# Kernel optimization log

Hardware: AMD Instinct MI355X
Metric: run time of the kernel (lower is better)

## Reference

```python
import jax, jax.numpy as jnp
import numpy as np

N_COARSE = 262145   # GMGN self.n
K_LEVELS = 5        # self.k
M_NBR = 9           # self.m
HID = 2048          # hidden_channels


def _build_grid():
    # replicates GMGN.init_toep_kernel (mtype='toep_mg')
    n_fine = 2 * (N_COARSE - 1) + 1          # 524289
    x = np.linspace(-1.0, 1.0, n_fine)
    x_lst, idx_lst = [], []
    for _ in range(K_LEVELS):
        n = x.shape[0]
        idx = np.arange((n - 1) // 2 - M_NBR + 1, (n - 1) // 2 + M_NBR)[1::2]  # m-1 center pts
        idx_lst.append(idx)
        x_lst.append(x[idx])
        x = x[::2]                            # injection1d
    x_lst.append(x)                           # coarse grid
    xs = np.concatenate(x_lst)[:, None].astype(np.float32)   # (N_eval, 1)
    nbrs = np.stack(idx_lst[::-1]).astype(np.int64)          # (k, m-1), coarse->fine
    return xs, nbrs


def setup_inputs() -> dict:
    key = jax.random.key(0)
    xs_np, nbrs_np = _build_grid()
    dims = [1, HID, HID, HID, HID, 1]
    inp = {"xs": jnp.asarray(xs_np), "nbrs": jnp.asarray(nbrs_np), "k": K_LEVELS, "m": M_NBR}
    ks = jax.random.split(key, 10)
    for j in range(5):
        bd = 1.0 / np.sqrt(dims[j])           # nn.Linear default init range
        inp[f"w{j}"] = jax.random.uniform(ks[2 * j], (dims[j], dims[j + 1]), jnp.float32, -bd, bd)
        inp[f"b{j}"] = jax.random.uniform(ks[2 * j + 1], (dims[j + 1],), jnp.float32, -bd, bd)
    return inp


def _interp1d(a):
    # linear prolongation: (n,) -> (2n-1,); even slots copy, odd slots average
    out = jnp.zeros((2 * a.shape[0] - 1,), a.dtype)
    out = out.at[0::2].set(a)
    return out.at[1::2].set(0.5 * (a[:-1] + a[1:]))


def _forward(xs, Ws, bs, nbrs, k, m):
    h = xs
    for W, b in zip(Ws, bs):
        h = jax.nn.relu(h @ W + b)            # MLP appends relu after every Linear (incl. last)
    Amg = h[:, 0]                             # (N_eval,) pointwise kernel values
    band = m - 1
    Abands = [Amg[band * i: band * (i + 1)] for i in range(k)][::-1]
    Ah = Amg[band * k:]                       # coarse kernel, length (n0-1)/2^k + 1
    for i in range(k):
        Ah = _interp1d(Ah)                    # upsample one level
        Ah = Ah.at[nbrs[i]].set(Abands[i])    # overwrite center band with exact MLP evals
    return Ah[None, None]                     # (1, 1, 2*(n-1)+1)


def reference(xs, w0, b0, w1, b1, w2, b2, w3, b3, w4, b4, nbrs, k, m):
    return _forward(xs, (w0, w1, w2, w3, w4), (b0, b1, b2, b3, b4), nbrs, k, m)
```

## Files before the change

### kernel.cpp

```cpp
#include <hip/hip_runtime.h>
#include <stdint.h>

#define HID    2048
#define MPTS   16425
#define MTILES 129
#define NTIL   16
#define KTIL   64
#define BIMG   5120

typedef float    f32x4 __attribute__((ext_vector_type(4)));
typedef _Float16 f16x8 __attribute__((ext_vector_type(8)));


__global__ void pack_w16(const float* __restrict__ w1,
                         const float* __restrict__ w2,
                         const float* __restrict__ w3,
                         _Float16* __restrict__ wp) {
    const int kt = blockIdx.x, nt = blockIdx.y, L = blockIdx.z;
    const float* W = (L == 0) ? w1 : ((L == 1) ? w2 : w3);
    __shared__ float tl[128 * 33];
    const int tid = threadIdx.x;
    const int k  = tid >> 3;
    const int nc = (tid & 7) * 16;
    const float* src = W + (size_t)(kt * 32 + k) * HID + nt * 128 + nc;
    #pragma unroll
    for (int j = 0; j < 16; ++j) tl[(nc + j) * 33 + k] = src[j];
    __syncthreads();
    const size_t base = (size_t)(L * 1024 + nt * 64 + kt) * BIMG;
    for (int e = tid; e < BIMG; e += 256) {
        int n = e / 40, kk = e - n * 40;
        wp[base + e] = (kk < 32) ? (_Float16)tl[n * 33 + kk] : (_Float16)0.f;
    }
}

__global__ void layer0p(const float* __restrict__ xs,
                        const float* __restrict__ w0,
                        const float* __restrict__ b0,
                        _Float16* __restrict__ Ahg,
                        _Float16* __restrict__ Alg, int row0) {
    const int r = blockIdx.x;
    const int grow = row0 + r;
    const int j0 = threadIdx.x * 8;
    const float x = (grow < MPTS) ? xs[grow] : 0.f;
    f16x8 h, l;
    #pragma unroll
    for (int q = 0; q < 8; ++q) {
        float v = x * w0[j0 + q] + b0[j0 + q];
        v = v > 0.f ? v : 0.f;
        _Float16 hs = (_Float16)v;
        h[q] = hs;
        l[q] = (_Float16)(v - (float)hs);
    }
    const int t = r >> 7, rowgrp = (r >> 4) & 7, lidx = r & 15;
    const int kt = j0 >> 5, quad = (j0 >> 3) & 3;
    const size_t dst = ((size_t)(t * 64 + kt) << 12) + rowgrp * 512 + quad * 128 + lidx * 8;
    *(f16x8*)(Ahg + dst) = h;
    *(f16x8*)(Alg + dst) = l;
}

__launch_bounds__(256, 3)
__global__ void gemm_hl(const _Float16* __restrict__ Ahg,
                        const _Float16* __restrict__ Alg,
                        const _Float16* __restrict__ wp,
                        const float* __restrict__ bias,
                        _Float16* __restrict__ Chg,
                        _Float16* __restrict__ Clg,
                        int layer, int write_lo,
                        float* __restrict__ Amg4,
                        const float* __restrict__ w4g, int row0) {
    __shared__ _Float16 Bs[4][BIMG];

    const int tid  = threadIdx.x;
    const int lane = tid & 63;
    const int wave = tid >> 6;
    const int quad = lane >> 4;
    const int lidx = lane & 15;

    const int nwg = (int)(gridDim.x * gridDim.y);
    const int L   = (int)(blockIdx.y * gridDim.x + blockIdx.x);
    const int F   = (L & 7) * (nwg >> 3) + (L >> 3);
    const int nt  = F & 15;
    const int mt  = F >> 4;

    const int mbase = wave * 32;

    const char* gW = (const char*)(wp + (size_t)(layer * 1024 + nt * 64) * BIMG);

    const size_t abase = ((size_t)(mt * 64) << 12) + (size_t)(mbase >> 4) * 512 + (size_t)lane * 8;
    const _Float16* aH = Ahg + abase;
    const _Float16* aL = Alg + abase;

    f32x4 acc[2][8];
    #pragma unroll
    for (int i = 0; i < 2; ++i)
        #pragma unroll
        for (int j = 0; j < 8; ++j) acc[i][j] = (f32x4)0.f;

#define PF_B(KT, BUF) do {                                                            \
    const char* nW_ = gW + (size_t)(KT) * (BIMG * 2);                                 \
    char* dW_ = (char*)&Bs[BUF][0];                                                   \
    for (int t = wave; t < 10; t += 4) {                                              \
        __builtin_amdgcn_global_load_lds(                                             \
            (const __attribute__((address_space(1))) unsigned int*)(nW_ + t * 1024 + lane * 16), \
            (__attribute__((address_space(3))) unsigned int*)(dW_ + t * 1024), 16, 0, 0); \
    }                                                                                 \
} while (0)

#define LD_A(KT, H, Lo) do {                                                          \
    const size_t ak_ = (size_t)(KT) << 12;                                            \
    _Pragma("unroll")                                                                 \
    for (int mm = 0; mm < 2; ++mm) {                                                  \
        H[mm]  = *(const f16x8*)(aH + ak_ + mm * 512);                                \
        Lo[mm] = *(const f16x8*)(aL + ak_ + mm * 512);                                \
    }                                                                                 \
} while (0)

#define LD_B(BUF, BF) do {                                                            \
    _Pragma("unroll")                                                                 \
    for (int nn = 0; nn < 8; ++nn) {                                                  \
        int r_ = nn * 16 + lidx;                                                      \
        BF[nn] = *(const f16x8*)(&Bs[BUF][r_ * 40 + quad * 8]);                       \
    }                                                                                 \
} while (0)

#define MFMA32(AH, AL, BF) do {                                                       \
    _Pragma("unroll")                                                                 \
    for (int mm = 0; mm < 2; ++mm)                                                    \
        _Pragma("unroll")                                                             \
        for (int nn = 0; nn < 8; ++nn) {                                              \
            acc[mm][nn] = __builtin_amdgcn_mfma_f32_16x16x32_f16(AH[mm], BF[nn], acc[mm][nn], 0, 0, 0); \
            acc[mm][nn] = __builtin_amdgcn_mfma_f32_16x16x32_f16(AL[mm], BF[nn], acc[mm][nn], 0, 0, 0); \
        }                                                                             \
} while (0)

#define GATE4() do {                                                                  \
    asm volatile("s_waitcnt vmcnt(4)" ::: "memory");                                  \
    __builtin_amdgcn_sched_barrier(0);                                                \
    __builtin_amdgcn_s_barrier();                                                     \
    __builtin_amdgcn_sched_barrier(0);                                                \
} while (0)

#define SUPER(S, P, DO_PF, DO_A2) do {                                                \
    f16x8 bfr0_[8];                                                                   \
    LD_B(2 * (P), bfr0_);                                                             \
    if (DO_PF) { PF_B(2 * (S) + 2, 2 * ((P) ^ 1)); PF_B(2 * (S) + 3, 2 * ((P) ^ 1) + 1); } \
    LD_A(2 * (S) + 1, nah, nal);                                                      \
    MFMA32(cah, cal, bfr0_);                                                          \
    f16x8 bfr1_[8];                                                                   \
    LD_B(2 * (P) + 1, bfr1_);                                                         \
    if (DO_A2) LD_A(2 * (S) + 2, cah, cal);                                           \
    MFMA32(nah, nal, bfr1_);                                                          \
    GATE4();                                                                          \
} while (0)

    f16x8 cah[2], cal[2], nah[2], nal[2];

    PF_B(0, 0);
    PF_B(1, 1);
    LD_A(0, cah, cal);
    __syncthreads();

    for (int ss = 0; ss < 15; ++ss) {
        SUPER(2 * ss,     0, 1, 1);
        SUPER(2 * ss + 1, 1, 1, 1);
    }
    SUPER(30, 0, 1, 1);
    SUPER(31, 1, 0, 0);

#undef SUPER
#undef GATE4
#undef MFMA32
#undef LD_B
#undef LD_A
#undef PF_B

    if (Amg4) {
        float w4v[8], bv[8];
        #pragma unroll
        for (int nn = 0; nn < 8; ++nn) {
            const int col = nt * 128 + nn * 16 + lidx;
            w4v[nn] = w4g[col];
            bv[nn]  = bias[col];
        }
        #pragma unroll
        for (int mm = 0; mm < 2; ++mm) {
            #pragma unroll
            for (int r = 0; r < 4; ++r) {
                float p = 0.f;
                #pragma unroll
                for (int nn = 0; nn < 8; ++nn) {
                    float v = acc[mm][nn][r] + bv[nn];
                    v = v > 0.f ? v : 0.f;
                    p += v * w4v[nn];
                }
                #pragma unroll
                for (int off = 1; off <= 8; off <<= 1)
                    p += __shfl_xor(p, off, 16);
                if (lidx == 0) {
                    const int grow = row0 + mt * 128 + mbase + mm * 16 + quad * 4 + r;
                    if (grow < MPTS) atomicAdd(Amg4 + grow, p);
                }
            }
        }
        return;
    }

    #pragma unroll
    for (int nn = 0; nn < 8; ++nn) {
        const int col = nt * 128 + nn * 16 + lidx;
        const float bv = bias[col];
        const int kt2 = col >> 5, quad2 = (col >> 3) & 3, j2 = col & 7;
        const size_t cb = ((size_t)(mt * 64 + kt2) << 12) + quad2 * 128 + j2;
        #pragma unroll
        for (int mm = 0; mm < 2; ++mm) {
            const int rowg = (mbase >> 4) + mm;
            #pragma unroll
            for (int r = 0; r < 4; ++r) {
                const int lidx2 = quad * 4 + r;
                float v = acc[mm][nn][r] + bv;
                v = v > 0.f ? v : 0.f;
                _Float16 hs = (_Float16)v;
                const size_t idx = cb + rowg * 512 + lidx2 * 8;
                Chg[idx] = hs;
                if (write_lo) Clg[idx] = (_Float16)(v - (float)hs);
            }
        }
    }
}

__global__ void layer0f(const float* __restrict__ xs, const float* __restrict__ w0,
                        const float* __restrict__ b0, float* __restrict__ A, int row0) {
    const int r = blockIdx.x;
    const int j = threadIdx.x * 8;
    const float x = (row0 + r < MPTS) ? xs[row0 + r] : 0.f;
    float* out = A + (size_t)r * HID + j;
    #pragma unroll
    for (int q = 0; q < 8; ++q) {
        float v = x * w0[j + q] + b0[j + q];
        out[q] = v > 0.f ? v : 0.f;
    }
}

__launch_bounds__(256)
__global__ void gemm_valu(const float* __restrict__ A, const float* __restrict__ W,
                          const float* __restrict__ bias, float* __restrict__ C) {
    __shared__ float As[16][132];
    __shared__ float Ws[16][132];
    const int tid = threadIdx.x;
    const int tx = tid & 15, ty = tid >> 4;
    const int n0 = blockIdx.x * 128;
    const int m0 = blockIdx.y * 128;
    const int am = tid & 127, ak = (tid >> 7) * 8;
    const int wn = (tid & 15) * 8, wk = tid >> 4;
    const float* aptr = A + (size_t)(m0 + am) * HID + ak;
    const float* wptr = W + (size_t)wk * HID + n0 + wn;
    float acc[8][8];
    #pragma unroll
    for (int i = 0; i < 8; ++i)
        #pragma unroll
        for (int j = 0; j < 8; ++j) acc[i][j] = 0.f;
    for (int k0 = 0; k0 < HID; k0 += 16) {
        f32x4 a0 = *(const f32x4*)(aptr + k0);
        f32x4 a1 = *(const f32x4*)(aptr + k0 + 4);
        f32x4 w0v = *(const f32x4*)(wptr + (size_t)k0 * HID);
        f32x4 w1v = *(const f32x4*)(wptr + (size_t)k0 * HID + 4);
        __syncthreads();
        As[ak + 0][am] = a0[0]; As[ak + 1][am] = a0[1];
        As[ak + 2][am] = a0[2]; As[ak + 3][am] = a0[3];
        As[ak + 4][am] = a1[0]; As[ak + 5][am] = a1[1];
        As[ak + 6][am] = a1[2]; As[ak + 7][am] = a1[3];
        *(f32x4*)&Ws[wk][wn]     = w0v;
        *(f32x4*)&Ws[wk][wn + 4] = w1v;
        __syncthreads();
        #pragma unroll
        for (int kk = 0; kk < 16; ++kk) {
            f32x4 av0 = *(const f32x4*)&As[kk][ty * 8];
            f32x4 av1 = *(const f32x4*)&As[kk][ty * 8 + 4];
            f32x4 bv0 = *(const f32x4*)&Ws[kk][tx * 8];
            f32x4 bv1 = *(const f32x4*)&Ws[kk][tx * 8 + 4];
            float a[8] = {av0[0], av0[1], av0[2], av0[3], av1[0], av1[1], av1[2], av1[3]};
            float b[8] = {bv0[0], bv0[1], bv0[2], bv0[3], bv1[0], bv1[1], bv1[2], bv1[3]};
            #pragma unroll
            for (int i = 0; i < 8; ++i)
                #pragma unroll
                for (int j = 0; j < 8; ++j) acc[i][j] += a[i] * b[j];
        }
    }
    #pragma unroll
    for (int i = 0; i < 8; ++i) {
        const int m = m0 + ty * 8 + i;
        #pragma unroll
        for (int jc = 0; jc < 2; ++jc) {
            const int n = n0 + tx * 8 + jc * 4;
            f32x4 v4;
            #pragma unroll
            for (int q = 0; q < 4; ++q) {
                float v = acc[i][jc * 4 + q] + bias[n + q];
                v4[q] = v > 0.f ? v : 0.f;
            }
            *(f32x4*)(C + (size_t)m * HID + n) = v4;
        }
    }
}

__global__ void layer4f(const float* __restrict__ A, const float* __restrict__ w4,
                        const float* __restrict__ b4, float* __restrict__ Amg, int row0) {
    const int lane = threadIdx.x & 63;
    const int wave = threadIdx.x >> 6;
    const int r    = blockIdx.x * 4 + wave;
    if (row0 + r >= MPTS) return;
    const float* ap = A + (size_t)r * HID;
    float s = 0.f;
    #pragma unroll
    for (int c = 0; c < 8; ++c) {
        const int col = c * 256 + lane * 4;
        f32x4 av = *(const f32x4*)(ap + col);
        f32x4 wv = *(const f32x4*)(w4 + col);
        s += av[0] * wv[0] + av[1] * wv[1] + av[2] * wv[2] + av[3] * wv[3];
    }
    #pragma unroll
    for (int off = 32; off; off >>= 1) s += __shfl_down(s, off);
    if (lane == 0) {
        float v = s + b4[0];
        Amg[row0 + r] = v > 0.f ? v : 0.f;
    }
}

__global__ void mg_level(const float* __restrict__ in, float* __restrict__ outf,
                         const int* __restrict__ nbrs_base, int level,
                         const float* __restrict__ band, int n_out,
                         const float* __restrict__ b4p, int xin) {
    const int j = blockIdx.x * 256 + threadIdx.x;
    if (j >= n_out) return;
    const float b4v = b4p ? b4p[0] : 0.f;
    float v;
    if (j & 1) {
        float a = in[j >> 1], b = in[(j >> 1) + 1];
        if (xin) { a = fmaxf(a + b4v, 0.f); b = fmaxf(b + b4v, 0.f); }
        v = 0.5f * (a + b);
    } else {
        float a = in[j >> 1];
        if (xin) a = fmaxf(a + b4v, 0.f);
        v = a;
    }
    const int stride =
        (nbrs_base[1] == 0 && nbrs_base[3] == 0 && nbrs_base[5] == 0) ? 2 : 1;
    #pragma unroll
    for (int t = 0; t < 8; ++t) {
        const int idx = nbrs_base[(level * 8 + t) * stride];
        if (j == idx) {
            float bb = band[t];
            if (b4p) bb = fmaxf(bb + b4v, 0.f);
            v = bb;
        }
    }
    outf[j] = v;
}

extern "C" void kernel_launch(void* const* d_in, const int* in_sizes, int n_in,
                              void* d_out, int out_size, void* d_ws, size_t ws_size,
                              hipStream_t stream) {
    int iXS=0, iNB=1, iW0=4, iB0=5, iW1=6, iB1=7, iW2=8, iB2=9,
        iW3=10, iB3=11, iW4=12, iB4=13;
    if (n_in >= 14) {
        if (in_sizes[0] == HID) {
            iB0=0; iB1=1; iB2=2; iB3=3; iB4=4; iNB=7;
            iW0=8; iW1=9; iW2=10; iW3=11; iW4=12; iXS=13;
        } else if (!(in_sizes[1] == 40 || in_sizes[1] == 80)) {
            iXS=0; iW0=1; iB0=2; iW1=3; iB1=4; iW2=5; iB2=6;
            iW3=7; iB3=8; iW4=9; iB4=10; iNB=11;
        }
    }
    const float* xs = (const float*)d_in[iXS];
    const int* nbrs = (const int*)d_in[iNB];
    const float* w0 = (const float*)d_in[iW0];
    const float* b0 = (const float*)d_in[iB0];
    const float* w1 = (const float*)d_in[iW1];
    const float* b1 = (const float*)d_in[iB1];
    const float* w2 = (const float*)d_in[iW2];
    const float* b2 = (const float*)d_in[iB2];
    const float* w3 = (const float*)d_in[iW3];
    const float* b3 = (const float*)d_in[iB3];
    const float* w4 = (const float*)d_in[iW4];
    const float* b4 = (const float*)d_in[iB4];

    char* ws = (char*)d_ws;
    const size_t szAmg = 66048;
    const size_t szAh1 = 524544;
    const size_t szAh2 = 1048832;
    float* Amg = (float*)(ws);
    float* ahA = (float*)(ws + szAmg);
    float* ahB = (float*)(ws + szAmg + szAh1);
    const size_t casc_end = szAmg + szAh1 + szAh2;
    const size_t szW    = (size_t)3 * 1024 * BIMG * 2;
    const size_t per_tile = 2ull * 128 * HID * 4;

    const int use_mfma = (ws_size >= casc_end + szW + per_tile) ? 1 : 0;

    _Float16* wp = (_Float16*)(ws + casc_end);
    const size_t buf_start = use_mfma ? (casc_end + szW) : casc_end;

    size_t avail = ws_size - buf_start;
    int CT = (int)(avail / per_tile);
    if (CT < 1) CT = 1;
    if (CT > 96) CT = 96;

    if (use_mfma) {
        const size_t half = (size_t)CT * 128 * HID;
        _Float16* bAh = (_Float16*)(ws + buf_start);
        _Float16* bAl = bAh + half;
        _Float16* bBh = bAh + 2 * half;
        _Float16* bBl = bAh + 3 * half;

        hipMemsetAsync(Amg, 0, (size_t)MPTS * sizeof(float), stream);

        pack_w16<<<dim3(KTIL, NTIL, 3), 256, 0, stream>>>(w1, w2, w3, wp);

        for (int t0 = 0; t0 < MTILES; t0 += CT) {
            int tiles = (MTILES - t0 < CT) ? (MTILES - t0) : CT;
            int row0 = t0 * 128;
            layer0p<<<dim3(tiles * 128), 256, 0, stream>>>(xs, w0, b0, bAh, bAl, row0);
            dim3 ggrid(NTIL, tiles);
            gemm_hl<<<ggrid, 256, 0, stream>>>(bAh, bAl, wp, b1, bBh, bBl, 0, 1,
                                               nullptr, nullptr, 0);
            gemm_hl<<<ggrid, 256, 0, stream>>>(bBh, bBl, wp, b2, bAh, bAl, 1, 1,
                                               nullptr, nullptr, 0);
            gemm_hl<<<ggrid, 256, 0, stream>>>(bAh, bAl, wp, b3, bBh, bBl, 2, 0,
                                               Amg, w4, row0);
        }
    } else {
        float* bufA = (float*)(ws + buf_start);
        float* bufB = (float*)(ws + buf_start + (size_t)CT * 128 * HID * 4);
        for (int t0 = 0; t0 < MTILES; t0 += CT) {
            int tiles = (MTILES - t0 < CT) ? (MTILES - t0) : CT;
            int row0 = t0 * 128;
            layer0f<<<dim3(tiles * 128), 256, 0, stream>>>(xs, w0, b0, bufA, row0);
            dim3 ggrid(NTIL, tiles);
            gemm_valu<<<ggrid, 256, 0, stream>>>(bufA, w1, b1, bufB);
            gemm_valu<<<ggrid, 256, 0, stream>>>(bufB, w2, b2, bufA);
            gemm_valu<<<ggrid, 256, 0, stream>>>(bufA, w3, b3, bufB);
            layer4f<<<dim3(tiles * 32), 256, 0, stream>>>(bufB, w4, b4, Amg, row0);
        }
    }

    const float* b4p = use_mfma ? b4 : nullptr;
    const float* cur = Amg + 40;
    float* dsts[5] = {ahA, ahB, ahA, ahB, (float*)d_out};
    int n = 16385;
    for (int i = 0; i < 5; ++i) {
        int n_out = 2 * n - 1;
        mg_level<<<dim3((n_out + 255) / 256), 256, 0, stream>>>(
            cur, dsts[i], nbrs, i, Amg + 8 * (4 - i), n_out,
            b4p, (i == 0 && use_mfma) ? 1 : 0);
        cur = dsts[i];
        n = n_out;
    }
    (void)out_size;
}
```

Before: 914.6 us.

## Fuse layer-0 pointwise MLP into first MFMA GEMM and raise tile cap

Removes the separate layer0p kernel and instead computes relu(x*w0+b0) split into fp16 hi/lo fragments in registers inside a new gemm_f0 kernel, feeding them straight into the MFMA loop for layer 1. This avoids writing and re-reading the 129-tile activation buffer for layer 0 and saves a kernel launch per chunk. The chunk cap is raised from 96 to all 129 tiles so the work can run in fewer, larger launches if workspace allows. In exchange there is extra VALU work per k-step, recomputed in every N-tile block, and more register pressure.

Result: faster. 893.8 us (-2.3%).

```diff
diff --git a/kernel.cpp b/kernel.cpp
--- a/kernel.cpp
+++ b/kernel.cpp
@@ -31,31 +31,6 @@
         int n = e / 40, kk = e - n * 40;
         wp[base + e] = (kk < 32) ? (_Float16)tl[n * 33 + kk] : (_Float16)0.f;
     }
-}
-
-__global__ void layer0p(const float* __restrict__ xs,
-                        const float* __restrict__ w0,
-                        const float* __restrict__ b0,
-                        _Float16* __restrict__ Ahg,
-                        _Float16* __restrict__ Alg, int row0) {
-    const int r = blockIdx.x;
-    const int grow = row0 + r;
-    const int j0 = threadIdx.x * 8;
-    const float x = (grow < MPTS) ? xs[grow] : 0.f;
-    f16x8 h, l;
-    #pragma unroll
-    for (int q = 0; q < 8; ++q) {
-        float v = x * w0[j0 + q] + b0[j0 + q];
-        v = v > 0.f ? v : 0.f;
-        _Float16 hs = (_Float16)v;
-        h[q] = hs;
-        l[q] = (_Float16)(v - (float)hs);
-    }
-    const int t = r >> 7, rowgrp = (r >> 4) & 7, lidx = r & 15;
-    const int kt = j0 >> 5, quad = (j0 >> 3) & 3;
-    const size_t dst = ((size_t)(t * 64 + kt) << 12) + rowgrp * 512 + quad * 128 + lidx * 8;
-    *(f16x8*)(Ahg + dst) = h;
-    *(f16x8*)(Alg + dst) = l;
 }
 
 __launch_bounds__(256, 3)
@@ -228,6 +203,169 @@
     }
 }
 
+__launch_bounds__(256, 3)
+__global__ void gemm_f0(const float* __restrict__ xs,
+                        const float* __restrict__ w0f,
+                        const float* __restrict__ b0f,
+                        const _Float16* __restrict__ wp,
+                        const float* __restrict__ bias,
+                        _Float16* __restrict__ Chg,
+                        _Float16* __restrict__ Clg, int row0) {
+    __shared__ _Float16 Bs[4][BIMG];
+
+    const int tid  = threadIdx.x;
+    const int lane = tid & 63;
+    const int wave = tid >> 6;
+    const int quad = lane >> 4;
+    const int lidx = lane & 15;
+
+    const int nwg = (int)(gridDim.x * gridDim.y);
+    const int L   = (int)(blockIdx.y * gridDim.x + blockIdx.x);
+    const int F   = (L & 7) * (nwg >> 3) + (L >> 3);
+    const int nt  = F & 15;
+    const int mt  = F >> 4;
+
+    const int mbase = wave * 32;
+
+    const char* gW = (const char*)(wp + (size_t)(nt * 64) * BIMG);
+
+    const int g0 = row0 + mt * 128 + mbase + lidx;
+    const float x0 = (g0 < MPTS) ? xs[g0] : 0.f;
+    const float x1 = (g0 + 16 < MPTS) ? xs[g0 + 16] : 0.f;
+
+    f32x4 acc[2][8];
+    #pragma unroll
+    for (int i = 0; i < 2; ++i)
+        #pragma unroll
+        for (int j = 0; j < 8; ++j) acc[i][j] = (f32x4)0.f;
+
+#define PF0(KT, BUF) do {                                                             \
+    const char* nW_ = gW + (size_t)(KT) * (BIMG * 2);                                 \
+    char* dW_ = (char*)&Bs[BUF][0];                                                   \
+    for (int t = wave; t < 10; t += 4) {                                              \
+        __builtin_amdgcn_global_load_lds(                                             \
+            (const __attribute__((address_space(1))) unsigned int*)(nW_ + t * 1024 + lane * 16), \
+            (__attribute__((address_space(3))) unsigned int*)(dW_ + t * 1024), 16, 0, 0); \
+    }                                                                                 \
+} while (0)
+
+#define LDW0(KT, WA, WB, BA, BB) do {                                                 \
+    const int k0_ = (KT) * 32 + quad * 8;                                             \
+    WA = *(const f32x4*)(w0f + k0_);                                                  \
+    WB = *(const f32x4*)(w0f + k0_ + 4);                                              \
+    BA = *(const f32x4*)(b0f + k0_);                                                  \
+    BB = *(const f32x4*)(b0f + k0_ + 4);                                              \
+} while (0)
+
+#define COMP0(WA, WB, BA, BB) do {                                                    \
+    _Pragma("unroll")                                                                 \
+    for (int mm = 0; mm < 2; ++mm) {                                                  \
+        const float xm_ = mm ? x1 : x0;                                               \
+        f16x8 h_, l_;                                                                 \
+        _Pragma("unroll")                                                             \
+        for (int j = 0; j < 4; ++j) {                                                 \
+            float v_ = xm_ * WA[j] + BA[j];                                           \
+            v_ = v_ > 0.f ? v_ : 0.f;                                                 \
+            _Float16 hs_ = (_Float16)v_;                                              \
+            h_[j] = hs_; l_[j] = (_Float16)(v_ - (float)hs_);                         \
+        }                                                                             \
+        _Pragma("unroll")                                                             \
+        for (int j = 0; j < 4; ++j) {                                                 \
+            float v_ = xm_ * WB[j] + BB[j];                                           \
+            v_ = v_ > 0.f ? v_ : 0.f;                                                 \
+            _Float16 hs_ = (_Float16)v_;                                              \
+            h_[4 + j] = hs_; l_[4 + j] = (_Float16)(v_ - (float)hs_);                 \
+        }                                                                             \
+        cah[mm] = h_; cal[mm] = l_;                                                   \
+    }                                                                                 \
+} while (0)
+
+#define LDB0(BUF, BF) do {                                                            \
+    _Pragma("unroll")                                                                 \
+    for (int nn = 0; nn < 8; ++nn) {                                                  \
+        int r_ = nn * 16 + lidx;                                                      \
+        BF[nn] = *(const f16x8*)(&Bs[BUF][r_ * 40 + quad * 8]);                       \
+    }                                                                                 \
+} while (0)
+
+#define MFMA0(BF) do {                                                                \
+    _Pragma("unroll")                                                                 \
+    for (int mm = 0; mm < 2; ++mm)                                                    \
+        _Pragma("unroll")                                                             \
+        for (int nn = 0; nn < 8; ++nn) {                                              \
+            acc[mm][nn] = __builtin_amdgcn_mfma_f32_16x16x32_f16(cah[mm], BF[nn], acc[mm][nn], 0, 0, 0); \
+            acc[mm][nn] = __builtin_amdgcn_mfma_f32_16x16x32_f16(cal[mm], BF[nn], acc[mm][nn], 0, 0, 0); \
+        }                                                                             \
+} while (0)
+
+#define GATE0() do {                                                                  \
+    asm volatile("s_waitcnt vmcnt(4)" ::: "memory");                                  \
+    __builtin_amdgcn_sched_barrier(0);                                                \
+    __builtin_amdgcn_s_barrier();                                                     \
+    __builtin_amdgcn_sched_barrier(0);                                                \
+} while (0)
+
+#define SUPERF(S, P, DO_PF, DO_W2) do {                                               \
+    f16x8 bfr0_[8];                                                                   \
+    LDB0(2 * (P), bfr0_);                                                             \
+    if (DO_PF) { PF0(2 * (S) + 2, 2 * ((P) ^ 1)); PF0(2 * (S) + 3, 2 * ((P) ^ 1) + 1); } \
+    LDW0(2 * (S) + 1, wBa, wBb, bBa, bBb);                                            \
+    COMP0(wAa, wAb, bAa, bAb);                                             \
+    MFMA0(bfr0_);                                                                     \
+    f16x8 bfr1_[8];                                                                   \
+    LDB0(2 * (P) + 1, bfr1_);                                                         \
+    if (DO_W2) LDW0(2 * (S) + 2, wAa, wAb, bAa, bAb);                                 \
+    COMP0(wBa, wBb, bBa, bBb);             \
+    MFMA0(bfr1_);                                                                     \
+    GATE0();                                 \
+} while (0)
+
+    f16x8 cah[2], cal[2];
+    f32x4 wAa, wAb, bAa, bAb, wBa, wBb, bBa, bBb;
+
+    PF0(0, 0);
+    PF0(1, 1);
+    LDW0(0, wAa, wAb, bAa, bAb);
+    __syncthreads();
+
+    for (int ss = 0; ss < 15; ++ss) {
+        SUPERF(2 * ss,     0, 1, 1);
+        SUPERF(2 * ss + 1, 1, 1, 1);
+    }
+    SUPERF(30, 0, 1, 1);
+    SUPERF(31, 1, 0, 0);
+
+#undef SUPERF
+#undef GATE0
+#undef MFMA0
+#undef LDB0
+#undef COMP0
+#undef LDW0
+#undef PF0
+
+    #pragma unroll
+    for (int nn = 0; nn < 8; ++nn) {
+        const int col = nt * 128 + nn * 16 + lidx;
+        const float bv = bias[col];
+        const int kt2 = col >> 5, quad2 = (col >> 3) & 3, j2 = col & 7;
+        const size_t cb = ((size_t)(mt * 64 + kt2) << 12) + quad2 * 128 + j2;
+        #pragma unroll
+        for (int mm = 0; mm < 2; ++mm) {
+            const int rowg = (mbase >> 4) + mm;
+            #pragma unroll
+            for (int r = 0; r < 4; ++r) {
+                const int lidx2 = quad * 4 + r;
+                float v = acc[mm][nn][r] + bv;
+                v = v > 0.f ? v : 0.f;
+                _Float16 hs = (_Float16)v;
+                const size_t idx = cb + rowg * 512 + lidx2 * 8;
+                Chg[idx] = hs;
+                Clg[idx] = (_Float16)(v - (float)hs);
+            }
+        }
+    }
+}
+
 __global__ void layer0f(const float* __restrict__ xs, const float* __restrict__ w0,
                         const float* __restrict__ b0, float* __restrict__ A, int row0) {
     const int r = blockIdx.x;
@@ -403,7 +541,7 @@
     size_t avail = ws_size - buf_start;
     int CT = (int)(avail / per_tile);
     if (CT < 1) CT = 1;
-    if (CT > 96) CT = 96;
+    if (CT > MTILES) CT = MTILES;
 
     if (use_mfma) {
         const size_t half = (size_t)CT * 128 * HID;
@@ -419,10 +557,8 @@
         for (int t0 = 0; t0 < MTILES; t0 += CT) {
             int tiles = (MTILES - t0 < CT) ? (MTILES - t0) : CT;
             int row0 = t0 * 128;
-            layer0p<<<dim3(tiles * 128), 256, 0, stream>>>(xs, w0, b0, bAh, bAl, row0);
             dim3 ggrid(NTIL, tiles);
-            gemm_hl<<<ggrid, 256, 0, stream>>>(bAh, bAl, wp, b1, bBh, bBl, 0, 1,
-                                               nullptr, nullptr, 0);
+            gemm_f0<<<ggrid, 256, 0, stream>>>(xs, w0, b0, wp, b1, bBh, bBl, row0);
             gemm_hl<<<ggrid, 256, 0, stream>>>(bBh, bBl, wp, b2, bAh, bAl, 1, 1,
                                                nullptr, nullptr, 0);
             gemm_hl<<<ggrid, 256, 0, stream>>>(bAh, bAl, wp, b3, bBh, bBl, 2, 0,
```
